# Optimization experiments

Hardware: AMD Instinct MI355X
Metric: run time of the kernel (lower is better)

The kernel has to match this reference:

```python
import jax, jax.numpy as jnp
import numpy as np

B, S, HIDDEN = 2, 1024, 2048
N_HEADS, N_KV_HEADS, HEAD_DIM = 32, 8, 64
GROUP = N_HEADS // N_KV_HEADS  # 4
ROPE_THETA = 10000.0


def rotate_half(x):
    half = x.shape[-1] // 2
    return jnp.concatenate((-x[..., half:], x[..., :half]), axis=-1)


def setup_inputs() -> dict:
    key = jax.random.key(0)
    ks = jax.random.split(key, 5)
    hidden_state = jax.random.normal(ks[0], (B, S, HIDDEN), jnp.float32)
    attention_mask = jnp.ones((B, S), jnp.float32)
    # RoPE tables, shape (S, HEAD_DIM)
    inv_freq = 1.0 / (ROPE_THETA ** (jnp.arange(0, HEAD_DIM, 2, dtype=jnp.float32) / HEAD_DIM))
    freqs = jnp.outer(jnp.arange(S, dtype=jnp.float32), inv_freq)
    emb = jnp.concatenate([freqs, freqs], axis=-1)
    cos, sin = jnp.cos(emb), jnp.sin(emb)
    scale = 0.02
    wq = jax.random.normal(ks[1], (HIDDEN, N_HEADS * HEAD_DIM), jnp.float32) * scale
    wk = jax.random.normal(ks[2], (HIDDEN, N_KV_HEADS * HEAD_DIM), jnp.float32) * scale
    wv = jax.random.normal(ks[3], (HIDDEN, N_KV_HEADS * HEAD_DIM), jnp.float32) * scale
    wo = jax.random.normal(ks[4], (N_HEADS * HEAD_DIM, HIDDEN), jnp.float32) * scale
    return {"hidden_state": hidden_state, "attention_mask": attention_mask,
            "cos": cos, "sin": sin, "wq": wq, "wk": wk, "wv": wv, "wo": wo}


def reference(hidden_state, attention_mask, cos, sin, wq, wk, wv, wo):
    b, s, _ = hidden_state.shape

    def split_heads(x):  # (B,S,n*D) -> (n,B,S,D), matching movedim(-2, 0)
        return jnp.moveaxis(x.reshape(b, s, -1, HEAD_DIM), -2, 0)

    q = split_heads(hidden_state @ wq)   # (H, B, S, D)
    k = split_heads(hidden_state @ wk)   # (KV, B, S, D)
    v = split_heads(hidden_state @ wv)   # (KV, B, S, D)

    q = q * cos + rotate_half(q) * sin
    k = k * cos + rotate_half(k) * sin

    # GQA: repeat_interleave K/V heads to match query heads
    k = jnp.repeat(k, GROUP, axis=0)     # (H, B, S, D)
    v = jnp.repeat(v, GROUP, axis=0)

    scores = jnp.einsum('hbqd,hbkd->hbqk', q, k) / jnp.sqrt(jnp.float32(HEAD_DIM))

    # causal + padding mask bias: 0 where tril(mask)==1, -inf elsewhere
    m = jnp.tril(jnp.broadcast_to(attention_mask[:, None, :], (b, s, s)))  # (B,S,S)
    bias = jnp.where((1.0 - m) != 0.0, -jnp.inf, 0.0)
    scores = scores + bias               # (H,B,S,S) + (B,S,S)

    attn = jax.nn.softmax(scores, axis=-1)
    ctx = jnp.einsum('hbqk,hbkd->hbqd', attn, v)
    ctx = jnp.moveaxis(ctx, 0, -2).reshape(b, s, -1)  # (B,S,H*D)
    out = ctx @ wo
    return (out, jnp.swapaxes(attn, 0, 1))  # attention.transpose(0,1) -> (B,H,S,S)
```

## Files before the change

kernel.cpp:

```cpp
#include <hip/hip_runtime.h>


typedef unsigned short u16;
typedef unsigned char  u8;
typedef unsigned int   u32;
typedef __attribute__((ext_vector_type(4))) float  f32x4;
typedef __attribute__((ext_vector_type(8))) __bf16 bf16x8;

static __device__ __forceinline__ u16 f2b(float f) {
  u32 u = __builtin_bit_cast(u32, f);
  u = u + 0x7fffu + ((u >> 16) & 1u);
  return (u16)(u >> 16);
}

#define GLL16(gp, lp)                                                         \
  __builtin_amdgcn_global_load_lds(                                           \
      (__attribute__((address_space(1))) u32*)(gp),                           \
      (__attribute__((address_space(3))) u32*)(lp), 16, 0, 0)

__global__ __launch_bounds__(256) void cvt_kernel(const float* __restrict__ in,
                                                  u16* __restrict__ out, int n4) {
  int i = blockIdx.x * 256 + threadIdx.x;
  if (i >= n4) return;
  float4 v = ((const float4*)in)[i];
  ushort4 o;
  o.x = f2b(v.x); o.y = f2b(v.y); o.z = f2b(v.z); o.w = f2b(v.w);
  ((ushort4*)out)[i] = o;
}

__global__ __launch_bounds__(256) void tconv_kernel(const float* __restrict__ in,
                                                    u16* __restrict__ out,
                                                    int K, int N) {
  __shared__ float t[64][65];
  int k0 = blockIdx.x * 64, n0 = blockIdx.y * 64;
  int c = threadIdx.x & 63, r0 = threadIdx.x >> 6;
#pragma unroll
  for (int i = 0; i < 16; ++i) {
    int r = r0 + i * 4;
    t[r][c] = in[(size_t)(k0 + r) * N + n0 + c];
  }
  __syncthreads();
#pragma unroll
  for (int i = 0; i < 16; ++i) {
    int r = r0 + i * 4;
    out[(size_t)(n0 + r) * K + k0 + c] = f2b(t[c][r]);
  }
}

__global__ __launch_bounds__(256) void vtrans_kernel(const u16* __restrict__ vb,
                                                     u16* __restrict__ vt) {
  __shared__ u16 t[64][65];
  int s0 = blockIdx.x * 64;
  int g = blockIdx.y;
  int b = g >> 3, kvh = g & 7;
  int c = threadIdx.x & 63, r0 = threadIdx.x >> 6;
#pragma unroll
  for (int i = 0; i < 16; ++i) {
    int r = r0 + i * 4;
    t[r][c] = vb[(size_t)(b * 1024 + s0 + r) * 512 + kvh * 64 + c];
  }
  __syncthreads();
#pragma unroll
  for (int i = 0; i < 16; ++i) {
    int r = r0 + i * 4;
    vt[((size_t)g * 64 + r) * 1024 + s0 + c] = t[c][r];
  }
}

template <int EPI>
__global__ __launch_bounds__(256) void gemm_kernel(
    const u16* __restrict__ A, const u16* __restrict__ Bt, int K,
    u16* __restrict__ qb, u16* __restrict__ kb, u16* __restrict__ vb,
    float* __restrict__ out,
    const float* __restrict__ cosT, const float* __restrict__ sinT) {
  __shared__ u16 As[2][128 * 64];
  __shared__ u16 Bs[2][128 * 64];
  const int tid = threadIdx.x;
  const int w = tid >> 6, l = tid & 63;
  const int wr = w >> 1, wc = w & 1;
  const int lg = l >> 4, ll = l & 15;
  const int l8 = l >> 3, lc = l & 7;
  const int m0 = blockIdx.x * 128, n0 = blockIdx.y * 128;

  f32x4 acc[4][4] = {};

#define GSTAGE(KT, BUF)                                                       \
  {                                                                           \
    _Pragma("unroll")                                                         \
    for (int i = 0; i < 4; ++i) {                                             \
      int r0 = w * 32 + i * 8;                                                \
      int row = r0 + l8;                                                      \
      int cc = lc ^ (row & 7);                                                \
      GLL16(A  + (size_t)(m0 + row) * K + (KT) * 64 + cc * 8,                 \
            &As[BUF][r0 * 64]);                                               \
      GLL16(Bt + (size_t)(n0 + row) * K + (KT) * 64 + cc * 8,                 \
            &Bs[BUF][r0 * 64]);                                               \
    }                                                                         \
  }

  const int nkt = K >> 6;
  GSTAGE(0, 0);
  int cur = 0;
  for (int kt = 0; kt < nkt; ++kt) {
    __syncthreads();
    if (kt + 1 < nkt) GSTAGE(kt + 1, cur ^ 1);
#pragma unroll
    for (int kc = 0; kc < 2; ++kc) {
      int cblk = kc * 4 + lg;
      bf16x8 af[4], bfr[4];
#pragma unroll
      for (int mi = 0; mi < 4; ++mi) {
        int row = wr * 64 + mi * 16 + ll;
        af[mi] = *(const bf16x8*)&As[cur][row * 64 + ((cblk ^ (row & 7)) * 8)];
      }
#pragma unroll
      for (int ni = 0; ni < 4; ++ni) {
        int row = wc * 64 + ni * 16 + ll;
        bfr[ni] = *(const bf16x8*)&Bs[cur][row * 64 + ((cblk ^ (row & 7)) * 8)];
      }
#pragma unroll
      for (int mi = 0; mi < 4; ++mi)
#pragma unroll
        for (int ni = 0; ni < 4; ++ni)
          acc[mi][ni] = __builtin_amdgcn_mfma_f32_16x16x32_bf16(
              af[mi], bfr[ni], acc[mi][ni], 0, 0, 0);
    }
    cur ^= 1;
  }
#undef GSTAGE

  if constexpr (EPI == 0) {
    u16* dst; int ldc, c0;
    const bool dorope = (n0 < 2560);
    if (n0 < 2048)      { dst = qb; ldc = 2048; c0 = n0; }
    else if (n0 < 2560) { dst = kb; ldc = 512;  c0 = n0 - 2048; }
    else                { dst = vb; ldc = 512;  c0 = n0 - 2560; }
#pragma unroll
    for (int mi = 0; mi < 4; ++mi)
#pragma unroll
      for (int ni = 0; ni < 4; ++ni)
#pragma unroll
        for (int r = 0; r < 4; ++r) {
          int row = m0 + wr * 64 + mi * 16 + lg * 4 + r;
          int col = c0 + wc * 64 + ni * 16 + ll;
          float x = acc[mi][ni][r];
          if (dorope) {
            int d = ni * 16 + ll;
            int s = row & 1023;
            float cv = cosT[s * 64 + d], sv = sinT[s * 64 + d];
            float xp = acc[mi][ni ^ 2][r];
            x = (ni < 2) ? (x * cv - xp * sv) : (x * cv + xp * sv);
          }
          dst[(size_t)row * ldc + col] = f2b(x);
        }
  } else {
#pragma unroll
    for (int mi = 0; mi < 4; ++mi)
#pragma unroll
      for (int ni = 0; ni < 4; ++ni)
#pragma unroll
        for (int r = 0; r < 4; ++r) {
          int row = m0 + wr * 64 + mi * 16 + lg * 4 + r;
          int col = n0 + wc * 64 + ni * 16 + ll;
          out[(size_t)row * 2048 + col] = acc[mi][ni][r];
        }
  }
}

__global__ __launch_bounds__(256) void attn_kernel(
    const u16* __restrict__ Qb,
    const u16* __restrict__ Kb,
    const u16* __restrict__ Vt,
    const float* __restrict__ msk,
    float* __restrict__ attn,
    u16* __restrict__ ctx) {
  __shared__ u16 Ks[2][64 * 64];
  __shared__ u16 Vs[2][64 * 64];
  __shared__ float Ps[64 * 68];
  __shared__ u8 Msk[1024];

  const int tid = threadIdx.x, w = tid >> 6, l = tid & 63;
  const int lg = l >> 4, ll = l & 15;
  const int l8 = l >> 3, lc = l & 7;
  const int bid = blockIdx.x;
  const int qt1 = bid & 7;
  const int h = (bid >> 3) & 31;
  const int b = bid >> 8;
  const int kvh = h >> 2;

  for (int i = tid; i < 1024; i += 256) Msk[i] = (msk[b * 1024 + i] != 0.f);

#define STAGE_K(KT, BUF)                                                      \
  {                                                                           \
    for (int j = 0; j < 2; ++j) {                                             \
      int r0 = w * 16 + j * 8;                                                \
      int row = r0 + l8;                                                      \
      int cc = lc ^ (row & 7);                                                \
      GLL16(Kb + (size_t)(b * 1024 + (KT) * 64 + row) * 512 + kvh * 64 +      \
                cc * 8,                                                       \
            &Ks[BUF][r0 * 64]);                                               \
    }                                                                         \
  }
#define STAGE_V(KT, BUF)                                                      \
  {                                                                           \
    for (int j = 0; j < 2; ++j) {                                             \
      int r0 = w * 16 + j * 8;                                                \
      int row = r0 + l8;                                                      \
      int cc = lc ^ (row & 7);                                                \
      GLL16(Vt + (size_t)((b * 8 + kvh) * 64 + row) * 1024 + (KT) * 64 +      \
                cc * 8,                                                       \
            &Vs[BUF][r0 * 64]);                                               \
    }                                                                         \
  }

  for (int half = 0; half < 2; ++half) {
    const int qt = half ? (15 - qt1) : qt1;
    const int qrow0 = qt * 64 + w * 16 + lg * 4;

    bf16x8 qf[2];
    {
      const u16* qp = Qb + (size_t)(b * 1024 + qt * 64 + w * 16 + ll) * 2048 +
                      h * 64 + lg * 8;
      qf[0] = *(const bf16x8*)qp;
      qf[1] = *(const bf16x8*)(qp + 32);
    }

    __syncthreads();
    STAGE_K(0, 0);
    float l_r[4] = {0.f, 0.f, 0.f, 0.f};
    for (int kt = 0; kt <= qt; ++kt) {
      const int c = kt & 1;
      __syncthreads();
      if (kt < qt) STAGE_K(kt + 1, c ^ 1);
      f32x4 sc[4] = {};
#pragma unroll
      for (int kc = 0; kc < 2; ++kc) {
        int cblk = kc * 4 + lg;
#pragma unroll
        for (int ns = 0; ns < 4; ++ns) {
          int row = ns * 16 + ll;
          bf16x8 kf = *(const bf16x8*)&Ks[c][row * 64 + ((cblk ^ (row & 7)) * 8)];
          sc[ns] = __builtin_amdgcn_mfma_f32_16x16x32_bf16(qf[kc], kf, sc[ns], 0, 0, 0);
        }
      }
#pragma unroll
      for (int ns = 0; ns < 4; ++ns) {
        int col = kt * 64 + ns * 16 + ll;
        bool mb = Msk[col];
#pragma unroll
        for (int r = 0; r < 4; ++r) {
          float e = __expf(sc[ns][r] * 0.125f);
          l_r[r] += (mb && col <= qrow0 + r) ? e : 0.f;
        }
      }
    }
#pragma unroll
    for (int r = 0; r < 4; ++r) {
#pragma unroll
      for (int mm = 1; mm < 16; mm <<= 1) l_r[r] += __shfl_xor(l_r[r], mm, 64);
    }
    float rinv[4];
#pragma unroll
    for (int r = 0; r < 4; ++r) rinv[r] = 1.f / l_r[r];

    __syncthreads();
    STAGE_K(0, 0);
    STAGE_V(0, 0);
    f32x4 cacc[4] = {};
    for (int kt = 0; kt <= qt; ++kt) {
      const int c = kt & 1;
      __syncthreads();
      if (kt < qt) { STAGE_K(kt + 1, c ^ 1); STAGE_V(kt + 1, c ^ 1); }
      f32x4 sc[4] = {};
#pragma unroll
      for (int kc = 0; kc < 2; ++kc) {
        int cblk = kc * 4 + lg;
#pragma unroll
        for (int ns = 0; ns < 4; ++ns) {
          int row = ns * 16 + ll;
          bf16x8 kf = *(const bf16x8*)&Ks[c][row * 64 + ((cblk ^ (row & 7)) * 8)];
          sc[ns] = __builtin_amdgcn_mfma_f32_16x16x32_bf16(qf[kc], kf, sc[ns], 0, 0, 0);
        }
      }
#pragma unroll
      for (int ns = 0; ns < 4; ++ns) {
        int col = kt * 64 + ns * 16 + ll;
        bool mb = Msk[col];
#pragma unroll
        for (int r = 0; r < 4; ++r) {
          float e = __expf(sc[ns][r] * 0.125f) * rinv[r];
          float p = (mb && col <= qrow0 + r) ? e : 0.f;
          Ps[(w * 16 + lg * 4 + r) * 68 + ns * 16 + ll] = p;
        }
      }
      {
        size_t rowbase = ((size_t)((b * 32 + h) * 1024 + qt * 64 + w * 16));
#pragma unroll
        for (int rr = 0; rr < 4; ++rr) {
          int lr = rr * 4 + lg;
          f32x4 pv4 = *(const f32x4*)&Ps[(w * 16 + lr) * 68 + ll * 4];
          *(f32x4*)&attn[(rowbase + lr) * 1024 + kt * 64 + ll * 4] = pv4;
        }
      }
#pragma unroll
      for (int kc = 0; kc < 2; ++kc) {
        const float* pp = &Ps[(w * 16 + ll) * 68 + kc * 32 + lg * 8];
        f32x4 plo = *(const f32x4*)pp;
        f32x4 phi = *(const f32x4*)(pp + 4);
        bf16x8 pa;
        pa[0] = (__bf16)plo[0]; pa[1] = (__bf16)plo[1];
        pa[2] = (__bf16)plo[2]; pa[3] = (__bf16)plo[3];
        pa[4] = (__bf16)phi[0]; pa[5] = (__bf16)phi[1];
        pa[6] = (__bf16)phi[2]; pa[7] = (__bf16)phi[3];
        int cblk = kc * 4 + lg;
#pragma unroll
        for (int ns = 0; ns < 4; ++ns) {
          int row = ns * 16 + ll;
          bf16x8 vf = *(const bf16x8*)&Vs[c][row * 64 + ((cblk ^ (row & 7)) * 8)];
          cacc[ns] = __builtin_amdgcn_mfma_f32_16x16x32_bf16(pa, vf, cacc[ns], 0, 0, 0);
        }
      }
    }

#pragma unroll
    for (int ns = 0; ns < 4; ++ns)
#pragma unroll
      for (int r = 0; r < 4; ++r) {
        int tok = b * 1024 + qt * 64 + w * 16 + lg * 4 + r;
        ctx[(size_t)tok * 2048 + h * 64 + ns * 16 + ll] = f2b(cacc[ns][r]);
      }

    int c00 = (qt + 1) * 64;
    int nzf = (1024 - c00) >> 2;
    if (nzf > 0) {
      size_t rb = ((size_t)((b * 32 + h) * 1024 + qt * 64)) * 1024;
      for (int i = tid; i < 64 * nzf; i += 256) {
        int rr = i / nzf;
        int cc4 = i - rr * nzf;
        float4 z = make_float4(0.f, 0.f, 0.f, 0.f);
        *(float4*)&attn[rb + (size_t)rr * 1024 + c00 + (size_t)cc4 * 4] = z;
      }
    }
  }
#undef STAGE_K
#undef STAGE_V
}

extern "C" void kernel_launch(void* const* d_in, const int* in_sizes, int n_in,
                              void* d_out, int out_size, void* d_ws, size_t ws_size,
                              hipStream_t stream) {
  const float* hidden = (const float*)d_in[0];
  const float* mask   = (const float*)d_in[1];
  const float* cosT   = (const float*)d_in[2];
  const float* sinT   = (const float*)d_in[3];
  const float* wq     = (const float*)d_in[4];
  const float* wk     = (const float*)d_in[5];
  const float* wv     = (const float*)d_in[6];
  const float* wo     = (const float*)d_in[7];

  char* ws = (char*)d_ws;
  u16* hidbf = (u16*)(ws);
  u16* Wt    = (u16*)(ws + (8u << 20));
  u16* Qb    = (u16*)(ws + (20u << 20));
  u16* Kb    = (u16*)(ws + (28u << 20));
  u16* Vb    = (u16*)(ws + (30u << 20));
  u16* Vtg   = (u16*)(ws + (32u << 20));

  float* outp  = (float*)d_out;
  float* attnp = outp + (size_t)2 * 1024 * 2048;

  cvt_kernel<<<4096, 256, 0, stream>>>(hidden, hidbf, 1048576);
  tconv_kernel<<<dim3(32, 32), 256, 0, stream>>>(wq, Wt, 2048, 2048);
  tconv_kernel<<<dim3(32, 8), 256, 0, stream>>>(wk, Wt + (size_t)2048 * 2048, 2048, 512);
  tconv_kernel<<<dim3(32, 8), 256, 0, stream>>>(wv, Wt + (size_t)2560 * 2048, 2048, 512);
  gemm_kernel<0><<<dim3(16, 24), 256, 0, stream>>>(hidbf, Wt, 2048, Qb, Kb, Vb,
                                                   nullptr, cosT, sinT);
  vtrans_kernel<<<dim3(16, 16), 256, 0, stream>>>(Vb, Vtg);
  tconv_kernel<<<dim3(32, 32), 256, 0, stream>>>(wo, Wt, 2048, 2048);
  attn_kernel<<<512, 256, 0, stream>>>(Qb, Kb, Vtg, mask, attnp, hidbf);
  gemm_kernel<1><<<dim3(16, 16), 256, 0, stream>>>(hidbf, Wt, 2048,
                                                   nullptr, nullptr, nullptr, outp,
                                                   nullptr, nullptr);
}
```

Measured before the change: 464.4 us.

## Fuse prep conversions, write V transposed from GEMM epilogue, read V directly

All input conversions (hidden to bf16 and the four weight transposes) now run in a single prep kernel, and Wo gets its own buffer so it no longer has to wait for the QKV GEMM. The QKV GEMM epilogue writes V already transposed into the layout attention needs, which removes the separate vtrans kernel. The attention kernel stops staging V in shared memory and loads V fragments straight from global memory. This cuts launches, LDS use and one pass over V, but the direct global V reads may have higher latency and less coalescing than the LDS path.

New measurement: 484.6 us. 4.4% more time.

```diff
diff --git a/kernel.cpp b/kernel.cpp
--- a/kernel.cpp
+++ b/kernel.cpp
@@ -18,21 +18,28 @@
       (__attribute__((address_space(1))) u32*)(gp),                           \
       (__attribute__((address_space(3))) u32*)(lp), 16, 0, 0)
 
-__global__ __launch_bounds__(256) void cvt_kernel(const float* __restrict__ in,
-                                                  u16* __restrict__ out, int n4) {
-  int i = blockIdx.x * 256 + threadIdx.x;
-  if (i >= n4) return;
-  float4 v = ((const float4*)in)[i];
-  ushort4 o;
-  o.x = f2b(v.x); o.y = f2b(v.y); o.z = f2b(v.z); o.w = f2b(v.w);
-  ((ushort4*)out)[i] = o;
-}
-
-__global__ __launch_bounds__(256) void tconv_kernel(const float* __restrict__ in,
-                                                    u16* __restrict__ out,
-                                                    int K, int N) {
+__global__ __launch_bounds__(256) void prep_kernel(
+    const float* __restrict__ hidden, u16* __restrict__ hidbf,
+    const float* __restrict__ wq, const float* __restrict__ wk,
+    const float* __restrict__ wv, const float* __restrict__ wo,
+    u16* __restrict__ Wt, u16* __restrict__ Wo2) {
   __shared__ float t[64][65];
-  int k0 = blockIdx.x * 64, n0 = blockIdx.y * 64;
+  int blk = blockIdx.x;
+  if (blk < 4096) {
+    int i = blk * 256 + threadIdx.x;
+    float4 v = ((const float4*)hidden)[i];
+    ushort4 o;
+    o.x = f2b(v.x); o.y = f2b(v.y); o.z = f2b(v.z); o.w = f2b(v.w);
+    ((ushort4*)hidbf)[i] = o;
+    return;
+  }
+  blk -= 4096;
+  const float* in; u16* out; int N, nblk;
+  if (blk < 1024)      { in = wq; out = Wt;                       N = 2048; nblk = blk; }
+  else if (blk < 1280) { in = wk; out = Wt + (size_t)2048 * 2048; N = 512;  nblk = blk - 1024; }
+  else if (blk < 1536) { in = wv; out = Wt + (size_t)2560 * 2048; N = 512;  nblk = blk - 1280; }
+  else                 { in = wo; out = Wo2;                      N = 2048; nblk = blk - 1536; }
+  int k0 = (nblk & 31) * 64, n0 = (nblk >> 5) * 64;
   int c = threadIdx.x & 63, r0 = threadIdx.x >> 6;
 #pragma unroll
   for (int i = 0; i < 16; ++i) {
@@ -43,34 +50,14 @@
 #pragma unroll
   for (int i = 0; i < 16; ++i) {
     int r = r0 + i * 4;
-    out[(size_t)(n0 + r) * K + k0 + c] = f2b(t[c][r]);
-  }
-}
-
-__global__ __launch_bounds__(256) void vtrans_kernel(const u16* __restrict__ vb,
-                                                     u16* __restrict__ vt) {
-  __shared__ u16 t[64][65];
-  int s0 = blockIdx.x * 64;
-  int g = blockIdx.y;
-  int b = g >> 3, kvh = g & 7;
-  int c = threadIdx.x & 63, r0 = threadIdx.x >> 6;
-#pragma unroll
-  for (int i = 0; i < 16; ++i) {
-    int r = r0 + i * 4;
-    t[r][c] = vb[(size_t)(b * 1024 + s0 + r) * 512 + kvh * 64 + c];
-  }
-  __syncthreads();
-#pragma unroll
-  for (int i = 0; i < 16; ++i) {
-    int r = r0 + i * 4;
-    vt[((size_t)g * 64 + r) * 1024 + s0 + c] = t[c][r];
+    out[(size_t)(n0 + r) * 2048 + k0 + c] = f2b(t[c][r]);
   }
 }
 
 template <int EPI>
 __global__ __launch_bounds__(256) void gemm_kernel(
     const u16* __restrict__ A, const u16* __restrict__ Bt, int K,
-    u16* __restrict__ qb, u16* __restrict__ kb, u16* __restrict__ vb,
+    u16* __restrict__ qb, u16* __restrict__ kb, u16* __restrict__ vt,
     float* __restrict__ out,
     const float* __restrict__ cosT, const float* __restrict__ sinT) {
   __shared__ u16 As[2][128 * 64];
@@ -130,29 +117,42 @@
 #undef GSTAGE
 
   if constexpr (EPI == 0) {
-    u16* dst; int ldc, c0;
-    const bool dorope = (n0 < 2560);
-    if (n0 < 2048)      { dst = qb; ldc = 2048; c0 = n0; }
-    else if (n0 < 2560) { dst = kb; ldc = 512;  c0 = n0 - 2048; }
-    else                { dst = vb; ldc = 512;  c0 = n0 - 2560; }
-#pragma unroll
-    for (int mi = 0; mi < 4; ++mi)
-#pragma unroll
-      for (int ni = 0; ni < 4; ++ni)
-#pragma unroll
-        for (int r = 0; r < 4; ++r) {
-          int row = m0 + wr * 64 + mi * 16 + lg * 4 + r;
-          int col = c0 + wc * 64 + ni * 16 + ll;
-          float x = acc[mi][ni][r];
-          if (dorope) {
+    if (n0 >= 2560) {
+      const int cvbase = n0 - 2560;
+#pragma unroll
+      for (int mi = 0; mi < 4; ++mi)
+#pragma unroll
+        for (int ni = 0; ni < 4; ++ni) {
+          int cv = cvbase + wc * 64 + ni * 16 + ll;
+          int token0 = m0 + wr * 64 + mi * 16 + lg * 4;
+          int bb = token0 >> 10, s0 = token0 & 1023;
+          size_t drow = (size_t)(bb * 8 + (cv >> 6)) * 64 + (cv & 63);
+          ushort4 pk;
+          pk.x = f2b(acc[mi][ni][0]); pk.y = f2b(acc[mi][ni][1]);
+          pk.z = f2b(acc[mi][ni][2]); pk.w = f2b(acc[mi][ni][3]);
+          *(ushort4*)&vt[drow * 1024 + s0] = pk;
+        }
+    } else {
+      u16* dst; int ldc, c0;
+      if (n0 < 2048) { dst = qb; ldc = 2048; c0 = n0; }
+      else           { dst = kb; ldc = 512;  c0 = n0 - 2048; }
+#pragma unroll
+      for (int mi = 0; mi < 4; ++mi)
+#pragma unroll
+        for (int ni = 0; ni < 4; ++ni)
+#pragma unroll
+          for (int r = 0; r < 4; ++r) {
+            int row = m0 + wr * 64 + mi * 16 + lg * 4 + r;
+            int col = c0 + wc * 64 + ni * 16 + ll;
             int d = ni * 16 + ll;
             int s = row & 1023;
             float cv = cosT[s * 64 + d], sv = sinT[s * 64 + d];
+            float x  = acc[mi][ni][r];
             float xp = acc[mi][ni ^ 2][r];
             x = (ni < 2) ? (x * cv - xp * sv) : (x * cv + xp * sv);
+            dst[(size_t)row * ldc + col] = f2b(x);
           }
-          dst[(size_t)row * ldc + col] = f2b(x);
-        }
+    }
   } else {
 #pragma unroll
     for (int mi = 0; mi < 4; ++mi)
@@ -175,7 +175,6 @@
     float* __restrict__ attn,
     u16* __restrict__ ctx) {
   __shared__ u16 Ks[2][64 * 64];
-  __shared__ u16 Vs[2][64 * 64];
   __shared__ float Ps[64 * 68];
   __shared__ u8 Msk[1024];
 
@@ -187,6 +186,7 @@
   const int h = (bid >> 3) & 31;
   const int b = bid >> 8;
   const int kvh = h >> 2;
+  const u16* __restrict__ Vg = Vt + (size_t)((b * 8 + kvh) * 64) * 1024;
 
   for (int i = tid; i < 1024; i += 256) Msk[i] = (msk[b * 1024 + i] != 0.f);
 
@@ -201,17 +201,6 @@
             &Ks[BUF][r0 * 64]);                                               \
     }                                                                         \
   }
-#define STAGE_V(KT, BUF)                                                      \
-  {                                                                           \
-    for (int j = 0; j < 2; ++j) {                                             \
-      int r0 = w * 16 + j * 8;                                                \
-      int row = r0 + l8;                                                      \
-      int cc = lc ^ (row & 7);                                                \
-      GLL16(Vt + (size_t)((b * 8 + kvh) * 64 + row) * 1024 + (KT) * 64 +      \
-                cc * 8,                                                       \
-            &Vs[BUF][r0 * 64]);                                               \
-    }                                                                         \
-  }
 
   for (int half = 0; half < 2; ++half) {
     const int qt = half ? (15 - qt1) : qt1;
@@ -265,12 +254,11 @@
 
     __syncthreads();
     STAGE_K(0, 0);
-    STAGE_V(0, 0);
     f32x4 cacc[4] = {};
     for (int kt = 0; kt <= qt; ++kt) {
       const int c = kt & 1;
       __syncthreads();
-      if (kt < qt) { STAGE_K(kt + 1, c ^ 1); STAGE_V(kt + 1, c ^ 1); }
+      if (kt < qt) STAGE_K(kt + 1, c ^ 1);
       f32x4 sc[4] = {};
 #pragma unroll
       for (int kc = 0; kc < 2; ++kc) {
@@ -316,7 +304,7 @@
 #pragma unroll
         for (int ns = 0; ns < 4; ++ns) {
           int row = ns * 16 + ll;
-          bf16x8 vf = *(const bf16x8*)&Vs[c][row * 64 + ((cblk ^ (row & 7)) * 8)];
+          bf16x8 vf = *(const bf16x8*)&Vg[(size_t)row * 1024 + kt * 64 + cblk * 8];
           cacc[ns] = __builtin_amdgcn_mfma_f32_16x16x32_bf16(pa, vf, cacc[ns], 0, 0, 0);
         }
       }
@@ -343,7 +331,6 @@
     }
   }
 #undef STAGE_K
-#undef STAGE_V
 }
 
 extern "C" void kernel_launch(void* const* d_in, const int* in_sizes, int n_in,
@@ -361,24 +348,19 @@
   char* ws = (char*)d_ws;
   u16* hidbf = (u16*)(ws);
   u16* Wt    = (u16*)(ws + (8u << 20));
-  u16* Qb    = (u16*)(ws + (20u << 20));
-  u16* Kb    = (u16*)(ws + (28u << 20));
-  u16* Vb    = (u16*)(ws + (30u << 20));
-  u16* Vtg   = (u16*)(ws + (32u << 20));
+  u16* Wo2   = (u16*)(ws + (20u << 20));
+  u16* Qb    = (u16*)(ws + (28u << 20));
+  u16* Kb    = (u16*)(ws + (36u << 20));
+  u16* Vtg   = (u16*)(ws + (38u << 20));
 
   float* outp  = (float*)d_out;
   float* attnp = outp + (size_t)2 * 1024 * 2048;
 
-  cvt_kernel<<<4096, 256, 0, stream>>>(hidden, hidbf, 1048576);
-  tconv_kernel<<<dim3(32, 32), 256, 0, stream>>>(wq, Wt, 2048, 2048);
-  tconv_kernel<<<dim3(32, 8), 256, 0, stream>>>(wk, Wt + (size_t)2048 * 2048, 2048, 512);
-  tconv_kernel<<<dim3(32, 8), 256, 0, stream>>>(wv, Wt + (size_t)2560 * 2048, 2048, 512);
-  gemm_kernel<0><<<dim3(16, 24), 256, 0, stream>>>(hidbf, Wt, 2048, Qb, Kb, Vb,
+  prep_kernel<<<6656, 256, 0, stream>>>(hidden, hidbf, wq, wk, wv, wo, Wt, Wo2);
+  gemm_kernel<0><<<dim3(16, 24), 256, 0, stream>>>(hidbf, Wt, 2048, Qb, Kb, Vtg,
                                                    nullptr, cosT, sinT);
-  vtrans_kernel<<<dim3(16, 16), 256, 0, stream>>>(Vb, Vtg);
-  tconv_kernel<<<dim3(32, 32), 256, 0, stream>>>(wo, Wt, 2048, 2048);
   attn_kernel<<<512, 256, 0, stream>>>(Qb, Kb, Vtg, mask, attnp, hidbf);
-  gemm_kernel<1><<<dim3(16, 16), 256, 0, stream>>>(hidbf, Wt, 2048,
+  gemm_kernel<1><<<dim3(16, 16), 256, 0, stream>>>(hidbf, Wo2, 2048,
                                                    nullptr, nullptr, nullptr, outp,
                                                    nullptr, nullptr);
 }
```
